# Kernel optimization log

Measured on AMD Instinct MI355X. Metric: run time of the kernel, lower is better.

The kernel has to match this reference:

```python
import jax, jax.numpy as jnp
import numpy as np


def gru_step(x, h, Wih, Whh, bih, bhh):
    gi = x @ Wih.T + bih            # [N, 3H]
    gh = h @ Whh.T + bhh            # [N, 3H]
    ir, iz, inn = jnp.split(gi, 3, axis=-1)
    hr, hz, hn = jnp.split(gh, 3, axis=-1)
    r = jax.nn.sigmoid(ir + hr)
    z = jax.nn.sigmoid(iz + hz)
    n = jnp.tanh(inn + r * hn)
    return (1.0 - z) * n + z * h


def setup_inputs() -> dict:
    key = jax.random.key(0)
    ks = jax.random.split(key, 24)
    B, T, X, HE, HC = 8192, 30, 64, 256, 32
    s = 0.05
    rn = lambda k, shp: (jax.random.normal(k, shp, dtype=jnp.float32) * s)
    return {
        "batch_features": jax.random.normal(ks[0], (B, 2, T, X), dtype=jnp.float32),
        "coords": jax.random.uniform(ks[1], (B, T, 4), dtype=jnp.float32) * 100.0,
        "valid_mask": jax.random.bernoulli(ks[2], 0.8, (B, T)),
        # Event GRU (2 layers, input 64, hidden 256)
        "Wih0": rn(ks[3], (3 * HE, X)),  "Whh0": rn(ks[4], (3 * HE, HE)),
        "bih0": jnp.zeros((3 * HE,), jnp.float32), "bhh0": jnp.zeros((3 * HE,), jnp.float32),
        "Wih1": rn(ks[5], (3 * HE, HE)), "Whh1": rn(ks[6], (3 * HE, HE)),
        "bih1": jnp.zeros((3 * HE,), jnp.float32), "bhh1": jnp.zeros((3 * HE,), jnp.float32),
        # Coord GRU (1 layer, input 4, hidden 32)
        "WihC": rn(ks[7], (3 * HC, 4)), "WhhC": rn(ks[8], (3 * HC, HC)),
        "bihC": jnp.zeros((3 * HC,), jnp.float32), "bhhC": jnp.zeros((3 * HC,), jnp.float32),
        # Fusion module
        "We": rn(ks[9], (128, HE)), "be": jnp.zeros((128,), jnp.float32),
        "Wc": rn(ks[10], (128, HC)), "bc": jnp.zeros((128,), jnp.float32),
        "W1": rn(ks[11], (128, 256)), "b1": jnp.zeros((128,), jnp.float32),
        "W2": rn(ks[12], (2, 128)), "b2": jnp.zeros((2,), jnp.float32),
    }


def reference(batch_features, coords, valid_mask,
              Wih0, Whh0, bih0, bhh0, Wih1, Whh1, bih1, bhh1,
              WihC, WhhC, bihC, bhhC,
              We, be, Wc, bc, W1, b1, W2, b2):
    B, F, T, X = batch_features.shape  # F == 2 frames
    N = B * T
    HE = Whh0.shape[1]
    HC = WhhC.shape[1]
    # [B,2,T,X] -> [N,2,X]: per-track (prev, curr) feature sequence
    feats = jnp.transpose(batch_features, (0, 2, 1, 3)).reshape(N, F, X)
    h0 = jnp.zeros((N, HE), batch_features.dtype)
    h1 = jnp.zeros((N, HE), batch_features.dtype)
    for t in range(F):  # fixed 2-step unroll (n_frames=2)
        h0 = gru_step(feats[:, t], h0, Wih0, Whh0, bih0, bhh0)
        h1 = gru_step(h0, h1, Wih1, Whh1, bih1, bhh1)
    event_out = h1  # [N, 256] (dropout between GRU layers inactive in eval)
    # coord GRU: single step from zero state
    c = coords.reshape(N, 4)
    coord_out = gru_step(c, jnp.zeros((N, HC), coords.dtype), WihC, WhhC, bihC, bhhC)
    # fusion
    ep = event_out @ We.T + be          # [N,128]
    cp = coord_out @ Wc.T + bc          # [N,128]
    hid = jax.nn.relu(jnp.concatenate([ep, cp], axis=-1) @ W1.T + b1)
    logits = hid @ W2.T + b2            # [N,2]
    logits = logits.reshape(B, T, 2)
    # invalid tracks were skipped in the original; mask them to zero here
    return jnp.where(valid_mask[..., None], logits, 0.0)
```

## Files before the change

### kernel.cpp

```cpp
#include <hip/hip_runtime.h>


#define NROWS 245760
#define TT 30
#define KC 64

typedef __attribute__((ext_vector_type(4))) float f32x4;
typedef __attribute__((ext_vector_type(8))) short bf16x8;

__device__ __forceinline__ float bf2f(unsigned short u) {
    union { unsigned int u; float f; } v; v.u = ((unsigned int)u) << 16; return v.f;
}
__device__ __forceinline__ unsigned short f2bf(float f) {
    union { float f; unsigned int u; } v; v.f = f;
    unsigned int u = v.u;
    unsigned int r = u + 0x7fffu + ((u >> 16) & 1u);
    return (unsigned short)(r >> 16);
}
__device__ __forceinline__ float fexp2c(float x) {
    return __builtin_amdgcn_exp2f(fminf(x, 80.f));
}
__device__ __forceinline__ float fsigmoid(float x) {
    return __builtin_amdgcn_rcpf(1.f + fexp2c(-1.44269504f * x));
}
__device__ __forceinline__ float ftanh(float x) {
    float t = fexp2c(-2.88539008f * x);
    return (1.f - t) * __builtin_amdgcn_rcpf(1.f + t);
}
__device__ __forceinline__ f32x4 mfma16(bf16x8 a, bf16x8 b, f32x4 c) {
    return __builtin_amdgcn_mfma_f32_16x16x32_bf16(a, b, c, 0, 0, 0);
}
__device__ __forceinline__ void gload16(const unsigned short* g, unsigned short* l) {
    __builtin_amdgcn_global_load_lds(
        (const __attribute__((address_space(1))) void*)g,
        (__attribute__((address_space(3))) void*)l, 16, 0, 0);
}


__global__ void cvt_bf16(const float* __restrict__ src, unsigned short* __restrict__ dst, int n) {
    int i = blockIdx.x * 256 + threadIdx.x;
    if (i < n) dst[i] = f2bf(src[i]);
}

__global__ void bias_prep(const float* __restrict__ bih0, const float* __restrict__ bhh0, float* __restrict__ BC0,
                          const float* __restrict__ bih1, const float* __restrict__ bhh1, float* __restrict__ BC1) {
    int j = threadIdx.x;
    BC0[j]       = bih0[j]       + bhh0[j];
    BC0[256 + j] = bih0[256 + j] + bhh0[256 + j];
    BC0[512 + j] = bih0[512 + j];
    BC0[768 + j] = bhh0[512 + j];
    BC1[j]       = bih1[j]       + bhh1[j];
    BC1[256 + j] = bih1[256 + j] + bhh1[256 + j];
    BC1[512 + j] = bih1[512 + j];
    BC1[768 + j] = bhh1[512 + j];
}

__global__ void fuse_prep(const float* __restrict__ We, const float* __restrict__ be,
                          const float* __restrict__ Wc, const float* __restrict__ bc_,
                          const float* __restrict__ W1, const float* __restrict__ b1,
                          unsigned short* __restrict__ WF, float* __restrict__ BF) {
    int idx = blockIdx.x * 256 + threadIdx.x;
    if (idx >= 128 * 320) return;
    int o = idx / 320, k = idx - o * 320;
    float v = 0.f;
    if (k < 256) {
        for (int i = 0; i < 128; ++i) v += W1[o * 256 + i] * We[i * 256 + k];
    } else if (k < 288) {
        int kk = k - 256;
        for (int i = 0; i < 128; ++i) v += W1[o * 256 + 128 + i] * Wc[i * 32 + kk];
    }
    WF[o * 320 + k] = f2bf(v);
    if (k == 0) {
        float s = b1[o];
        for (int i = 0; i < 128; ++i) s += W1[o * 256 + i] * be[i];
        for (int i = 0; i < 128; ++i) s += W1[o * 256 + 128 + i] * bc_[i];
        BF[o] = s;
    }
}

__global__ void xprep(const float* __restrict__ bf, unsigned short* __restrict__ A1,
                      unsigned short* __restrict__ A3) {
    int i = blockIdx.x * 256 + threadIdx.x;
    int n = i >> 6, k = i & 63;
    int b = n / TT, t = n - b * TT;
    const float* p = bf + ((size_t)(b * 2) * TT + t) * 64 + k;
    A1[(size_t)n * 64 + k]  = f2bf(p[0]);
    A3[(size_t)n * 320 + k] = f2bf(p[TT * 64]);
}

__global__ void coord_gru(const float* __restrict__ coords, const float* __restrict__ WihC,
                          const float* __restrict__ bihC, const float* __restrict__ bhhC,
                          unsigned short* __restrict__ A5) {
    int n = blockIdx.x * 256 + threadIdx.x;
    if (n >= NROWS) return;
    const float4 c = *(const float4*)(coords + (size_t)n * 4);
    unsigned short* o = A5 + (size_t)n * 320 + 256;
    for (int j = 0; j < 32; ++j) {
        float gr = WihC[j * 4 + 0] * c.x + WihC[j * 4 + 1] * c.y + WihC[j * 4 + 2] * c.z + WihC[j * 4 + 3] * c.w + bihC[j];
        int j2 = 32 + j;
        float gz = WihC[j2 * 4 + 0] * c.x + WihC[j2 * 4 + 1] * c.y + WihC[j2 * 4 + 2] * c.z + WihC[j2 * 4 + 3] * c.w + bihC[j2];
        int j3 = 64 + j;
        float gn = WihC[j3 * 4 + 0] * c.x + WihC[j3 * 4 + 1] * c.y + WihC[j3 * 4 + 2] * c.z + WihC[j3 * 4 + 3] * c.w + bihC[j3];
        float r = fsigmoid(gr + bhhC[j]);
        float z = fsigmoid(gz + bhhC[j2]);
        float nn = ftanh(gn + r * bhhC[j3]);
        o[j] = f2bf((1.f - z) * nn);
    }
    for (int j = 32; j < 64; ++j) o[j] = 0;
}

__device__ __forceinline__ void gemm_phase(
    const unsigned short* __restrict__ Ag, int lda, int aoff, int Kp,
    const unsigned short* __restrict__ Wg,
    unsigned short* sA, unsigned short* sW,
    int row0, int cb, int tid,
    f32x4 (&aR)[2][4], f32x4 (&aZ)[2][4], f32x4 (&aG)[2][4]) {
    const int lane = tid & 63, wave = tid >> 6;
    const int lr = lane & 15, lk = lane >> 4;
    const int xr = (lr & 7) * 8;
    const int gsrc = ((lane & 7) ^ (lane >> 3)) * 8;
    const int lrow = lane >> 3;
    for (int kc = 0; kc < Kp; kc += KC) {
        __syncthreads();
#pragma unroll
        for (int it = 0; it < 4; ++it) {
            int grp = it * 4 + wave;
            const unsigned short* src = Ag + (size_t)(row0 + grp * 8 + lrow) * lda + aoff + kc + gsrc;
            gload16(src, sA + grp * 512);
        }
#pragma unroll
        for (int it = 0; it < 6; ++it) {
            int gw = it * 4 + wave;
            int t = gw >> 1;
            int c = (gw & 1) * 8 + lrow;
            int grow = (t >> 2) * 256 + cb * 64 + (t & 3) * 16 + c;
            const unsigned short* src = Wg + (size_t)grow * Kp + kc + gsrc;
            gload16(src, sW + gw * 512);
        }
        __syncthreads();
#pragma unroll
        for (int kk = 0; kk < 2; ++kk) {
            int kx = (kk * 32 + lk * 8) ^ xr;
            bf16x8 a0 = *(const bf16x8*)(sA + (wave * 32 + lr) * KC + kx);
            bf16x8 a1 = *(const bf16x8*)(sA + (wave * 32 + 16 + lr) * KC + kx);
#pragma unroll
            for (int t = 0; t < 12; ++t) {
                bf16x8 b = *(const bf16x8*)(sW + (t * 16 + lr) * KC + kx);
                int gi = t & 3;
                if (t < 4) {
                    aR[0][gi] = mfma16(a0, b, aR[0][gi]);
                    aR[1][gi] = mfma16(a1, b, aR[1][gi]);
                } else if (t < 8) {
                    aZ[0][gi] = mfma16(a0, b, aZ[0][gi]);
                    aZ[1][gi] = mfma16(a1, b, aZ[1][gi]);
                } else {
                    aG[0][gi] = mfma16(a0, b, aG[0][gi]);
                    aG[1][gi] = mfma16(a1, b, aG[1][gi]);
                }
            }
        }
    }
}

template <bool HAS_HH, bool HAS_HPREV>
__global__ __launch_bounds__(256, 3) void gru_gemm(
    const unsigned short* __restrict__ A, int lda,
    int Kih, const unsigned short* __restrict__ Wih,
    int Khh, const unsigned short* __restrict__ Whh,
    const float* __restrict__ bc,
    const unsigned short* __restrict__ hprev, int ldh,
    unsigned short* __restrict__ dst, int ldd) {
    __shared__ unsigned short sA[128 * KC];
    __shared__ unsigned short sW[192 * KC];
    const int tid = threadIdx.x;
    const int nwg = gridDim.x;
    const int wgid = (blockIdx.x & 7) * (nwg >> 3) + (blockIdx.x >> 3);
    const int cb = wgid & 3;
    const int row0 = (wgid >> 2) * 128;
    f32x4 aR[2][4] = {}, aZ[2][4] = {}, aIN[2][4] = {}, aHN[2][4] = {};
    gemm_phase(A, lda, 0, Kih, Wih, sA, sW, row0, cb, tid, aR, aZ, aIN);
    if (HAS_HH)
        gemm_phase(A, lda, Kih, Khh, Whh, sA, sW, row0, cb, tid, aR, aZ, aHN);
    const int lane = tid & 63, wave = tid >> 6;
    const int lr = lane & 15, lk = lane >> 4;
    const int jc = cb * 64;
    const int rb = row0 + wave * 32;
#pragma unroll
    for (int s = 0; s < 2; ++s) {
#pragma unroll
        for (int gi = 0; gi < 4; ++gi) {
            int j = jc + gi * 16 + lr;
            float br = bc[j], bz = bc[256 + j], bin = bc[512 + j], bhn = bc[768 + j];
#pragma unroll
            for (int q = 0; q < 4; ++q) {
                int row = rb + s * 16 + lk * 4 + q;
                float rg = fsigmoid(aR[s][gi][q] + br);
                float zg = fsigmoid(aZ[s][gi][q] + bz);
                float hn = HAS_HH ? aHN[s][gi][q] : 0.f;
                float ng = ftanh(aIN[s][gi][q] + bin + rg * (hn + bhn));
                float h = (1.f - zg) * ng;
                if (HAS_HPREV) h += zg * bf2f(hprev[(size_t)row * ldh + j]);
                dst[(size_t)row * ldd + j] = f2bf(h);
            }
        }
    }
}

__global__ __launch_bounds__(256, 3) void fusion_logits(
    const unsigned short* __restrict__ A,
    const unsigned short* __restrict__ WF,
    const float* __restrict__ BF, const float* __restrict__ W2, const float* __restrict__ b2,
    const int* __restrict__ mask, float* __restrict__ out) {
    __shared__ unsigned short sA[64 * KC];
    __shared__ unsigned short sW[128 * KC];
    const int tid = threadIdx.x, lane = tid & 63, wave = tid >> 6;
    const int lr = lane & 15, lk = lane >> 4;
    const int xr = (lr & 7) * 8;
    const int gsrc = ((lane & 7) ^ (lane >> 3)) * 8;
    const int lrow = lane >> 3;
    const int row0 = blockIdx.x * 64;
    f32x4 acc[8] = {};
    for (int kc = 0; kc < 320; kc += KC) {
        __syncthreads();
#pragma unroll
        for (int it = 0; it < 2; ++it) {
            int grp = it * 4 + wave;
            const unsigned short* src = A + (size_t)(row0 + grp * 8 + lrow) * 320 + kc + gsrc;
            gload16(src, sA + grp * 512);
        }
#pragma unroll
        for (int it = 0; it < 4; ++it) {
            int gw = it * 4 + wave;
            const unsigned short* src = WF + (size_t)(gw * 8 + lrow) * 320 + kc + gsrc;
            gload16(src, sW + gw * 512);
        }
        __syncthreads();
#pragma unroll
        for (int kk = 0; kk < 2; ++kk) {
            int kx = (kk * 32 + lk * 8) ^ xr;
            bf16x8 a = *(const bf16x8*)(sA + (wave * 16 + lr) * KC + kx);
#pragma unroll
            for (int t = 0; t < 8; ++t) {
                bf16x8 b = *(const bf16x8*)(sW + (t * 16 + lr) * KC + kx);
                acc[t] = mfma16(a, b, acc[t]);
            }
        }
    }
#pragma unroll
    for (int q = 0; q < 4; ++q) {
        float l0 = 0.f, l1 = 0.f;
#pragma unroll
        for (int t = 0; t < 8; ++t) {
            int j = t * 16 + lr;
            float h = acc[t][q] + BF[j];
            h = h > 0.f ? h : 0.f;
            l0 += h * W2[j];
            l1 += h * W2[128 + j];
        }
#pragma unroll
        for (int m = 1; m < 16; m <<= 1) {
            l0 += __shfl_xor(l0, m, 64);
            l1 += __shfl_xor(l1, m, 64);
        }
        if (lr == 0) {
            int row = row0 + wave * 16 + lk * 4 + q;
            float v0 = l0 + b2[0], v1 = l1 + b2[1];
            if (!mask[row]) { v0 = 0.f; v1 = 0.f; }
            out[(size_t)row * 2]     = v0;
            out[(size_t)row * 2 + 1] = v1;
        }
    }
}


extern "C" void kernel_launch(void* const* d_in, const int* in_sizes, int n_in,
                              void* d_out, int out_size, void* d_ws, size_t ws_size,
                              hipStream_t stream) {
    const float* bfeat  = (const float*)d_in[0];
    const float* coords = (const float*)d_in[1];
    const int* mask = (const int*)d_in[2];
    const float* Wih0 = (const float*)d_in[3];
    const float* Whh0 = (const float*)d_in[4];
    const float* bih0 = (const float*)d_in[5];
    const float* bhh0 = (const float*)d_in[6];
    const float* Wih1 = (const float*)d_in[7];
    const float* Whh1 = (const float*)d_in[8];
    const float* bih1 = (const float*)d_in[9];
    const float* bhh1 = (const float*)d_in[10];
    const float* WihC = (const float*)d_in[11];
    const float* bihC = (const float*)d_in[13];
    const float* bhhC = (const float*)d_in[14];
    const float* We = (const float*)d_in[15];
    const float* be = (const float*)d_in[16];
    const float* Wc = (const float*)d_in[17];
    const float* bc_ = (const float*)d_in[18];
    const float* W1 = (const float*)d_in[19];
    const float* b1 = (const float*)d_in[20];
    const float* W2 = (const float*)d_in[21];
    const float* b2 = (const float*)d_in[22];
    float* out = (float*)d_out;

    const size_t N = NROWS;
    char* ws = (char*)d_ws;
    unsigned short* A4 = (unsigned short*)ws;
    unsigned short* A1 = (unsigned short*)ws;
    unsigned short* A3 = (unsigned short*)(ws + N * 512 * 2);
    unsigned short* A5 = A3;
    char* wp = ws + N * 512 * 2 + N * 320 * 2;
    unsigned short* WB0  = (unsigned short*)wp; wp += 768 * 64 * 2;
    unsigned short* WBh0 = (unsigned short*)wp; wp += 768 * 256 * 2;
    unsigned short* WB1  = (unsigned short*)wp; wp += 768 * 256 * 2;
    unsigned short* WBh1 = (unsigned short*)wp; wp += 768 * 256 * 2;
    unsigned short* WF   = (unsigned short*)wp; wp += 128 * 320 * 2;
    float* BC0 = (float*)wp; wp += 1024 * 4;
    float* BC1 = (float*)wp; wp += 1024 * 4;
    float* BF  = (float*)wp; wp += 128 * 4;

    cvt_bf16<<<192, 256, 0, stream>>>(Wih0, WB0, 768 * 64);
    cvt_bf16<<<768, 256, 0, stream>>>(Whh0, WBh0, 768 * 256);
    cvt_bf16<<<768, 256, 0, stream>>>(Wih1, WB1, 768 * 256);
    cvt_bf16<<<768, 256, 0, stream>>>(Whh1, WBh1, 768 * 256);
    bias_prep<<<1, 256, 0, stream>>>(bih0, bhh0, BC0, bih1, bhh1, BC1);
    fuse_prep<<<160, 256, 0, stream>>>(We, be, Wc, bc_, W1, b1, WF, BF);
    xprep<<<61440, 256, 0, stream>>>(bfeat, A1, A3);

    const int gg = (NROWS / 128) * 4;
    gru_gemm<false, false><<<gg, 256, 0, stream>>>(A1, 64, 64, WB0, 0, nullptr, BC0, nullptr, 0, A3 + 64, 320);
    gru_gemm<false, false><<<gg, 256, 0, stream>>>(A3 + 64, 320, 256, WB1, 0, nullptr, BC1, nullptr, 0, A4 + 256, 512);
    gru_gemm<true, true><<<gg, 256, 0, stream>>>(A3, 320, 64, WB0, 256, WBh0, BC0, A3 + 64, 320, A4, 512);
    coord_gru<<<NROWS / 256, 256, 0, stream>>>(coords, WihC, bihC, bhhC, A5);
    gru_gemm<true, true><<<gg, 256, 0, stream>>>(A4, 512, 256, WB1, 256, WBh1, BC1, A4 + 256, 512, A5, 320);
    fusion_logits<<<NROWS / 64, 256, 0, stream>>>(A5, WF, BF, W2, b2, mask, out);

    (void)in_sizes; (void)n_in; (void)out_size; (void)ws_size;
}
```

Baseline: 791.0 us.

## Double-buffer LDS tiles in GRU and fusion GEMMs, vectorize input prep

The GRU GEMM and fusion kernels now keep two LDS buffers, so the global-to-LDS loads for the next K-chunk are issued before the MFMA work on the current chunk, with explicit vmcnt waits and barriers. The two GEMM phases (input and hidden weights) are merged into one pipelined loop. MFMA sections raise wave priority. xprep now uses float4 loads and 4-wide bf16 stores, and three weight conversion launches are merged into one. The doubled LDS footprint lowers the occupancy hint from 3 to 2 blocks per CU, which can reduce latency hiding.

```diff
diff --git a/kernel.cpp b/kernel.cpp
--- a/kernel.cpp
+++ b/kernel.cpp
@@ -7,6 +7,7 @@
 
 typedef __attribute__((ext_vector_type(4))) float f32x4;
 typedef __attribute__((ext_vector_type(8))) short bf16x8;
+typedef __attribute__((ext_vector_type(4))) unsigned short u16x4;
 
 __device__ __forceinline__ float bf2f(unsigned short u) {
     union { unsigned int u; float f; } v; v.u = ((unsigned int)u) << 16; return v.f;
@@ -40,6 +41,15 @@
 __global__ void cvt_bf16(const float* __restrict__ src, unsigned short* __restrict__ dst, int n) {
     int i = blockIdx.x * 256 + threadIdx.x;
     if (i < n) dst[i] = f2bf(src[i]);
+}
+
+__global__ void cvt3_bf16(const float* __restrict__ s0, const float* __restrict__ s1,
+                          const float* __restrict__ s2, unsigned short* __restrict__ d0,
+                          unsigned short* __restrict__ d1, unsigned short* __restrict__ d2) {
+    int i = blockIdx.x * 256 + threadIdx.x;
+    d0[i] = f2bf(s0[i]);
+    d1[i] = f2bf(s1[i]);
+    d2[i] = f2bf(s2[i]);
 }
 
 __global__ void bias_prep(const float* __restrict__ bih0, const float* __restrict__ bhh0, float* __restrict__ BC0,
@@ -81,11 +91,15 @@
 __global__ void xprep(const float* __restrict__ bf, unsigned short* __restrict__ A1,
                       unsigned short* __restrict__ A3) {
     int i = blockIdx.x * 256 + threadIdx.x;
-    int n = i >> 6, k = i & 63;
+    int n = i >> 4, q = i & 15;
     int b = n / TT, t = n - b * TT;
-    const float* p = bf + ((size_t)(b * 2) * TT + t) * 64 + k;
-    A1[(size_t)n * 64 + k]  = f2bf(p[0]);
-    A3[(size_t)n * 320 + k] = f2bf(p[TT * 64]);
+    const float* p = bf + ((size_t)(b * 2) * TT + t) * 64 + q * 4;
+    float4 v0 = *(const float4*)(p);
+    float4 v1 = *(const float4*)(p + TT * 64);
+    u16x4 o0 = { f2bf(v0.x), f2bf(v0.y), f2bf(v0.z), f2bf(v0.w) };
+    u16x4 o1 = { f2bf(v1.x), f2bf(v1.y), f2bf(v1.z), f2bf(v1.w) };
+    *(u16x4*)(A1 + (size_t)n * 64 + q * 4)  = o0;
+    *(u16x4*)(A3 + (size_t)n * 320 + q * 4) = o1;
 }
 
 __global__ void coord_gru(const float* __restrict__ coords, const float* __restrict__ WihC,
@@ -109,80 +123,105 @@
     for (int j = 32; j < 64; ++j) o[j] = 0;
 }
 
-__device__ __forceinline__ void gemm_phase(
-    const unsigned short* __restrict__ Ag, int lda, int aoff, int Kp,
-    const unsigned short* __restrict__ Wg,
-    unsigned short* sA, unsigned short* sW,
-    int row0, int cb, int tid,
+__device__ __forceinline__ void gemm_compute(
+    const unsigned short* sA, const unsigned short* sW,
+    int lr, int lk, int wave, int xr,
     f32x4 (&aR)[2][4], f32x4 (&aZ)[2][4], f32x4 (&aG)[2][4]) {
-    const int lane = tid & 63, wave = tid >> 6;
-    const int lr = lane & 15, lk = lane >> 4;
-    const int xr = (lr & 7) * 8;
-    const int gsrc = ((lane & 7) ^ (lane >> 3)) * 8;
-    const int lrow = lane >> 3;
-    for (int kc = 0; kc < Kp; kc += KC) {
-        __syncthreads();
-#pragma unroll
-        for (int it = 0; it < 4; ++it) {
-            int grp = it * 4 + wave;
-            const unsigned short* src = Ag + (size_t)(row0 + grp * 8 + lrow) * lda + aoff + kc + gsrc;
-            gload16(src, sA + grp * 512);
-        }
-#pragma unroll
-        for (int it = 0; it < 6; ++it) {
-            int gw = it * 4 + wave;
-            int t = gw >> 1;
-            int c = (gw & 1) * 8 + lrow;
-            int grow = (t >> 2) * 256 + cb * 64 + (t & 3) * 16 + c;
-            const unsigned short* src = Wg + (size_t)grow * Kp + kc + gsrc;
-            gload16(src, sW + gw * 512);
-        }
-        __syncthreads();
-#pragma unroll
-        for (int kk = 0; kk < 2; ++kk) {
-            int kx = (kk * 32 + lk * 8) ^ xr;
-            bf16x8 a0 = *(const bf16x8*)(sA + (wave * 32 + lr) * KC + kx);
-            bf16x8 a1 = *(const bf16x8*)(sA + (wave * 32 + 16 + lr) * KC + kx);
-#pragma unroll
-            for (int t = 0; t < 12; ++t) {
-                bf16x8 b = *(const bf16x8*)(sW + (t * 16 + lr) * KC + kx);
-                int gi = t & 3;
-                if (t < 4) {
-                    aR[0][gi] = mfma16(a0, b, aR[0][gi]);
-                    aR[1][gi] = mfma16(a1, b, aR[1][gi]);
-                } else if (t < 8) {
-                    aZ[0][gi] = mfma16(a0, b, aZ[0][gi]);
-                    aZ[1][gi] = mfma16(a1, b, aZ[1][gi]);
-                } else {
-                    aG[0][gi] = mfma16(a0, b, aG[0][gi]);
-                    aG[1][gi] = mfma16(a1, b, aG[1][gi]);
-                }
+    __builtin_amdgcn_s_setprio(1);
+#pragma unroll
+    for (int kk = 0; kk < 2; ++kk) {
+        int kx = (kk * 32 + lk * 8) ^ xr;
+        bf16x8 a0 = *(const bf16x8*)(sA + (wave * 32 + lr) * KC + kx);
+        bf16x8 a1 = *(const bf16x8*)(sA + (wave * 32 + 16 + lr) * KC + kx);
+#pragma unroll
+        for (int t = 0; t < 12; ++t) {
+            bf16x8 b = *(const bf16x8*)(sW + (t * 16 + lr) * KC + kx);
+            int gi = t & 3;
+            if (t < 4) {
+                aR[0][gi] = mfma16(a0, b, aR[0][gi]);
+                aR[1][gi] = mfma16(a1, b, aR[1][gi]);
+            } else if (t < 8) {
+                aZ[0][gi] = mfma16(a0, b, aZ[0][gi]);
+                aZ[1][gi] = mfma16(a1, b, aZ[1][gi]);
+            } else {
+                aG[0][gi] = mfma16(a0, b, aG[0][gi]);
+                aG[1][gi] = mfma16(a1, b, aG[1][gi]);
             }
         }
     }
+    __builtin_amdgcn_s_setprio(0);
 }
 
 template <bool HAS_HH, bool HAS_HPREV>
-__global__ __launch_bounds__(256, 3) void gru_gemm(
+__global__ __launch_bounds__(256, 2) void gru_gemm(
     const unsigned short* __restrict__ A, int lda,
     int Kih, const unsigned short* __restrict__ Wih,
     int Khh, const unsigned short* __restrict__ Whh,
     const float* __restrict__ bc,
     const unsigned short* __restrict__ hprev, int ldh,
     unsigned short* __restrict__ dst, int ldd) {
-    __shared__ unsigned short sA[128 * KC];
-    __shared__ unsigned short sW[192 * KC];
+    __shared__ unsigned short sA[2][128 * KC];
+    __shared__ unsigned short sW[2][192 * KC];
     const int tid = threadIdx.x;
     const int nwg = gridDim.x;
     const int wgid = (blockIdx.x & 7) * (nwg >> 3) + (blockIdx.x >> 3);
     const int cb = wgid & 3;
     const int row0 = (wgid >> 2) * 128;
-    f32x4 aR[2][4] = {}, aZ[2][4] = {}, aIN[2][4] = {}, aHN[2][4] = {};
-    gemm_phase(A, lda, 0, Kih, Wih, sA, sW, row0, cb, tid, aR, aZ, aIN);
-    if (HAS_HH)
-        gemm_phase(A, lda, Kih, Khh, Whh, sA, sW, row0, cb, tid, aR, aZ, aHN);
     const int lane = tid & 63, wave = tid >> 6;
     const int lr = lane & 15, lk = lane >> 4;
+    const int xr = (lr & 7) * 8;
+    const int gsrc = ((lane & 7) ^ (lane >> 3)) * 8;
+    const int lrow = lane >> 3;
+
+    const int nsteps0 = Kih >> 6;
+    const int nsteps = nsteps0 + (HAS_HH ? (Khh >> 6) : 0);
+
+    const unsigned short* pA[4];
+#pragma unroll
+    for (int it = 0; it < 4; ++it)
+        pA[it] = A + (size_t)(row0 + (it * 4 + wave) * 8 + lrow) * lda + gsrc;
+    const unsigned short* pWi[6];
+    const unsigned short* pWh[6];
+#pragma unroll
+    for (int it = 0; it < 6; ++it) {
+        int gw = it * 4 + wave;
+        int t = gw >> 1, c = (gw & 1) * 8 + lrow;
+        int grow = (t >> 2) * 256 + cb * 64 + (t & 3) * 16 + c;
+        pWi[it] = Wih + (size_t)grow * Kih + gsrc;
+        pWh[it] = HAS_HH ? (Whh + (size_t)grow * Khh + gsrc) : (Wih + gsrc);
+    }
+
+    f32x4 aR[2][4] = {}, aZ[2][4] = {}, aIN[2][4] = {}, aHN[2][4] = {};
+
+    auto STAGE = [&](int s, int b) {
+        const int acol = s * KC;
+        const bool sg1 = HAS_HH && (s >= nsteps0);
+        const int wcol = sg1 ? (s - nsteps0) * KC : acol;
+#pragma unroll
+        for (int it = 0; it < 4; ++it)
+            gload16(pA[it] + acol, &sA[b][(it * 4 + wave) * 512]);
+#pragma unroll
+        for (int it = 0; it < 6; ++it)
+            gload16((sg1 ? pWh[it] : pWi[it]) + wcol, &sW[b][(it * 4 + wave) * 512]);
+    };
+
+    STAGE(0, 0);
+    for (int s = 0; s < nsteps; ++s) {
+        const int b = s & 1;
+        if (s + 1 < nsteps) {
+            STAGE(s + 1, b ^ 1);
+            asm volatile("s_waitcnt vmcnt(10)" ::: "memory");
+        } else {
+            asm volatile("s_waitcnt vmcnt(0)" ::: "memory");
+        }
+        asm volatile("s_barrier" ::: "memory");
+        if (!HAS_HH || s < nsteps0)
+            gemm_compute(sA[b], sW[b], lr, lk, wave, xr, aR, aZ, aIN);
+        else
+            gemm_compute(sA[b], sW[b], lr, lk, wave, xr, aR, aZ, aHN);
+        asm volatile("s_barrier" ::: "memory");
+    }
+
     const int jc = cb * 64;
     const int rb = row0 + wave * 32;
 #pragma unroll
@@ -211,8 +250,8 @@
     const unsigned short* __restrict__ WF,
     const float* __restrict__ BF, const float* __restrict__ W2, const float* __restrict__ b2,
     const int* __restrict__ mask, float* __restrict__ out) {
-    __shared__ unsigned short sA[64 * KC];
-    __shared__ unsigned short sW[128 * KC];
+    __shared__ unsigned short sA[2][64 * KC];
+    __shared__ unsigned short sW[2][128 * KC];
     const int tid = threadIdx.x, lane = tid & 63, wave = tid >> 6;
     const int lr = lane & 15, lk = lane >> 4;
     const int xr = (lr & 7) * 8;
@@ -220,31 +259,48 @@
     const int lrow = lane >> 3;
     const int row0 = blockIdx.x * 64;
     f32x4 acc[8] = {};
-    for (int kc = 0; kc < 320; kc += KC) {
-        __syncthreads();
-#pragma unroll
-        for (int it = 0; it < 2; ++it) {
-            int grp = it * 4 + wave;
-            const unsigned short* src = A + (size_t)(row0 + grp * 8 + lrow) * 320 + kc + gsrc;
-            gload16(src, sA + grp * 512);
-        }
-#pragma unroll
-        for (int it = 0; it < 4; ++it) {
-            int gw = it * 4 + wave;
-            const unsigned short* src = WF + (size_t)(gw * 8 + lrow) * 320 + kc + gsrc;
-            gload16(src, sW + gw * 512);
-        }
-        __syncthreads();
+    const unsigned short* pA[2];
+#pragma unroll
+    for (int it = 0; it < 2; ++it)
+        pA[it] = A + (size_t)(row0 + (it * 4 + wave) * 8 + lrow) * 320 + gsrc;
+    const unsigned short* pW[4];
+#pragma unroll
+    for (int it = 0; it < 4; ++it)
+        pW[it] = WF + (size_t)((it * 4 + wave) * 8 + lrow) * 320 + gsrc;
+
+    auto STAGE = [&](int s, int b) {
+        const int col = s * KC;
+#pragma unroll
+        for (int it = 0; it < 2; ++it)
+            gload16(pA[it] + col, &sA[b][(it * 4 + wave) * 512]);
+#pragma unroll
+        for (int it = 0; it < 4; ++it)
+            gload16(pW[it] + col, &sW[b][(it * 4 + wave) * 512]);
+    };
+
+    STAGE(0, 0);
+    for (int s = 0; s < 5; ++s) {
+        const int b = s & 1;
+        if (s + 1 < 5) {
+            STAGE(s + 1, b ^ 1);
+            asm volatile("s_waitcnt vmcnt(6)" ::: "memory");
+        } else {
+            asm volatile("s_waitcnt vmcnt(0)" ::: "memory");
+        }
+        asm volatile("s_barrier" ::: "memory");
+        __builtin_amdgcn_s_setprio(1);
 #pragma unroll
         for (int kk = 0; kk < 2; ++kk) {
             int kx = (kk * 32 + lk * 8) ^ xr;
-            bf16x8 a = *(const bf16x8*)(sA + (wave * 16 + lr) * KC + kx);
+            bf16x8 a = *(const bf16x8*)(&sA[b][0] + (wave * 16 + lr) * KC + kx);
 #pragma unroll
             for (int t = 0; t < 8; ++t) {
-                bf16x8 b = *(const bf16x8*)(sW + (t * 16 + lr) * KC + kx);
-                acc[t] = mfma16(a, b, acc[t]);
+                bf16x8 bb = *(const bf16x8*)(&sW[b][0] + (t * 16 + lr) * KC + kx);
+                acc[t] = mfma16(a, bb, acc[t]);
             }
         }
+        __builtin_amdgcn_s_setprio(0);
+        asm volatile("s_barrier" ::: "memory");
     }
 #pragma unroll
     for (int q = 0; q < 4; ++q) {
@@ -317,12 +373,10 @@
     float* BF  = (float*)wp; wp += 128 * 4;
 
     cvt_bf16<<<192, 256, 0, stream>>>(Wih0, WB0, 768 * 64);
-    cvt_bf16<<<768, 256, 0, stream>>>(Whh0, WBh0, 768 * 256);
-    cvt_bf16<<<768, 256, 0, stream>>>(Wih1, WB1, 768 * 256);
-    cvt_bf16<<<768, 256, 0, stream>>>(Whh1, WBh1, 768 * 256);
+    cvt3_bf16<<<768, 256, 0, stream>>>(Whh0, Wih1, Whh1, WBh0, WB1, WBh1);
     bias_prep<<<1, 256, 0, stream>>>(bih0, bhh0, BC0, bih1, bhh1, BC1);
     fuse_prep<<<160, 256, 0, stream>>>(We, be, Wc, bc_, W1, b1, WF, BF);
-    xprep<<<61440, 256, 0, stream>>>(bfeat, A1, A3);
+    xprep<<<15360, 256, 0, stream>>>(bfeat, A1, A3);
 
     const int gg = (NROWS / 128) * 4;
     gru_gemm<false, false><<<gg, 256, 0, stream>>>(A1, 64, 64, WB0, 0, nullptr, BC0, nullptr, 0, A3 + 64, 320);
```

After: 2.735 ms. 3.46x slower.
